# Kernel tuning notes

Measured on AMD Instinct MI355X. Metric: run time of the kernel, lower is better.

Reference implementation:

```python
import jax, jax.numpy as jnp
import numpy as np

N = 50000       # nodes
E = 800000      # edges (avg degree 16)
H = 64          # hidden_channels
T = 4           # towers
F = H // T      # per-tower channels (divide_input=True) = 16
NAGG, NSC = 5, 3
# degree histogram passed as mol_deg -> avg log-degree scaler constant (as in PyG PNAConv)
MOL_DEG = np.array([0, 5, 15, 30, 25, 15, 7, 2, 1], dtype=np.float64)
_bins = np.arange(len(MOL_DEG))
AVG_LOG = float((np.log(_bins + 1.0) * MOL_DEG).sum() / MOL_DEG.sum())


def setup_inputs() -> dict:
    key = jax.random.key(0)
    ks = jax.random.split(key, 12)
    g = lambda k, shp, s=0.1: jax.random.normal(k, shp, dtype=jnp.float32) * s
    return {
        "atom_x": g(ks[0], (N, H), 1.0),
        "bond_emb": g(ks[1], (5, H)),                      # Embedding(5, H)
        "edge_w": g(ks[2], (H, F)), "edge_b": jnp.zeros((F,), jnp.float32),
        "pre_w1": g(ks[3], (T, 3 * F, F)), "pre_b1": jnp.zeros((T, F), jnp.float32),
        "pre_w2": g(ks[4], (T, F, F)), "pre_b2": jnp.zeros((T, F), jnp.float32),
        "post_w1": g(ks[5], (T, (1 + NAGG * NSC) * F, F)), "post_b1": jnp.zeros((T, F), jnp.float32),
        "post_w2": g(ks[6], (T, F, F)), "post_b2": jnp.zeros((T, F), jnp.float32),
        "lin_w": g(ks[7], (H, H)), "lin_b": jnp.zeros((H,), jnp.float32),
        "ln_g": jnp.ones((H,), jnp.float32), "ln_b": jnp.zeros((H,), jnp.float32),
        "bond_x": jax.random.randint(ks[8], (E,), 0, 5),
        "atom_edge_index": jax.random.randint(ks[9], (2, E), 0, N),
    }


def reference(atom_x, bond_emb, edge_w, edge_b, pre_w1, pre_b1, pre_w2, pre_b2,
              post_w1, post_b1, post_w2, post_b2, lin_w, lin_b, ln_g, ln_b,
              bond_x, atom_edge_index):
    src, dst = atom_edge_index[0], atom_edge_index[1]
    # bond encoder + PNA edge encoder (edge_dim -> F_in)
    e = bond_emb[bond_x] @ edge_w + edge_b                       # [E, F]
    xt = atom_x.reshape(N, T, F)                                 # divide_input
    x_j, x_i = xt[src], xt[dst]                                  # [E, T, F]
    et = jnp.broadcast_to(e[:, None, :], (E, T, F))
    h = jnp.concatenate([x_i, x_j, et], axis=-1)                 # [E, T, 3F]
    # per-tower pre-MLP (Linear -> ReLU -> Linear)
    h = jax.nn.relu(jnp.einsum('etf,tfg->etg', h, pre_w1) + pre_b1)
    h = jnp.einsum('etf,tfg->etg', h, pre_w2) + pre_b2           # messages [E, T, F]

    s = jax.ops.segment_sum(h, dst, num_segments=N)
    cnt = jax.ops.segment_sum(jnp.ones((E,), h.dtype), dst, num_segments=N)
    cnt_c = jnp.maximum(cnt, 1.0)[:, None, None]
    mean = s / cnt_c
    mean2 = jax.ops.segment_sum(h * h, dst, num_segments=N) / cnt_c
    std = jnp.sqrt(jax.nn.relu(mean2 - mean * mean) + 1e-5)
    has = (cnt > 0)[:, None, None]
    mn = jnp.where(has, jax.ops.segment_min(h, dst, num_segments=N), 0.0)
    mx = jnp.where(has, jax.ops.segment_max(h, dst, num_segments=N), 0.0)
    agg = jnp.concatenate([s, mean, mn, mx, std], axis=-1)       # [N, T, 5F]

    # degree scalers (deg clamped to 1, as in PyG DegreeScalerAggregation)
    ld = jnp.log(jnp.maximum(cnt, 1.0) + 1.0)[:, None, None]
    agg = jnp.concatenate([agg, agg * (ld / AVG_LOG), agg * (AVG_LOG / ld)], axis=-1)  # [N, T, 15F]

    out = jnp.concatenate([xt, agg], axis=-1)                    # [N, T, 16F]
    # per-tower post-MLP, then mix towers with final Linear
    out = jax.nn.relu(jnp.einsum('ntf,tfg->ntg', out, post_w1) + post_b1)
    out = jnp.einsum('ntf,tfg->ntg', out, post_w2) + post_b2     # [N, T, F]
    out = out.reshape(N, H) @ lin_w + lin_b                      # [N, H]

    # LayerNorm + ReLU + residual (dropout is identity in eval)
    mu = out.mean(-1, keepdims=True)
    var = out.var(-1, keepdims=True)
    ln = (out - mu) / jnp.sqrt(var + 1e-5) * ln_g + ln_b
    return atom_x + jax.nn.relu(ln)
```

## Files before the change

### kernel.cpp

```cpp
#include <hip/hip_runtime.h>
#include <cstdint>

typedef unsigned short u16;

#define AVG_LOG_F 1.4862356961977451f
#define MAXD 64

#define OFF_W2   3072
#define OFF_PW1  4096
#define OFF_PW2  20480
#define OFF_LW   21504
#define OFF_PB1  25600
#define OFF_PB2  25664
#define OFF_QB1  25728
#define OFF_QB2  25792
#define OFF_LB   25856
#define OFF_LG   25920
#define OFF_LBN  25984
#define OFF_EWT  26128
#define IB       26448

__device__ __forceinline__ float bf2f(u16 u) {
    return __uint_as_float(((unsigned)u) << 16);
}
__device__ __forceinline__ u16 f2bf(float f) {
    unsigned u = __float_as_uint(f);
    u += 0x7fffu + ((u >> 16) & 1u);
    return (u16)(u >> 16);
}
__device__ __forceinline__ float rdin(const void* p, long j, int mode) {
    if (mode == 0) return bf2f(((const u16*)p)[j]);
    return ((const float*)p)[j];
}
template <int MODE>
__device__ __forceinline__ void load16c(const void* p, long base, float* o) {
    if (MODE == 0) {
        const u16* q = (const u16*)p + base;
        uint4 a = *(const uint4*)q;
        uint4 b = *(const uint4*)(q + 8);
        o[0]  = __uint_as_float(a.x << 16); o[1]  = __uint_as_float(a.x & 0xffff0000u);
        o[2]  = __uint_as_float(a.y << 16); o[3]  = __uint_as_float(a.y & 0xffff0000u);
        o[4]  = __uint_as_float(a.z << 16); o[5]  = __uint_as_float(a.z & 0xffff0000u);
        o[6]  = __uint_as_float(a.w << 16); o[7]  = __uint_as_float(a.w & 0xffff0000u);
        o[8]  = __uint_as_float(b.x << 16); o[9]  = __uint_as_float(b.x & 0xffff0000u);
        o[10] = __uint_as_float(b.y << 16); o[11] = __uint_as_float(b.y & 0xffff0000u);
        o[12] = __uint_as_float(b.z << 16); o[13] = __uint_as_float(b.z & 0xffff0000u);
        o[14] = __uint_as_float(b.w << 16); o[15] = __uint_as_float(b.w & 0xffff0000u);
    } else {
        const float* q = (const float*)p + base;
        float4 a = *(const float4*)q;
        float4 b = *(const float4*)(q + 4);
        float4 c = *(const float4*)(q + 8);
        float4 d = *(const float4*)(q + 12);
        o[0]=a.x; o[1]=a.y; o[2]=a.z; o[3]=a.w;
        o[4]=b.x; o[5]=b.y; o[6]=b.z; o[7]=b.w;
        o[8]=c.x; o[9]=c.y; o[10]=c.z; o[11]=c.w;
        o[12]=d.x; o[13]=d.y; o[14]=d.z; o[15]=d.w;
    }
}

template <int MODE>
__device__ __forceinline__ void y_loop(const void* ax, const void* pre_w1, float* wsY, float* wsXW,
                                       int Nn, int wave, int nwaves, int l) {
    const int t = l >> 4, g = l & 15;
    float wxi[16], wxj[16];
#pragma unroll
    for (int f = 0; f < 16; f++) {
        wxi[f] = rdin(pre_w1, t * 768 + f * 16 + g, MODE);
        wxj[f] = rdin(pre_w1, t * 768 + (16 + f) * 16 + g, MODE);
    }
    for (int n = wave; n < Nn; n += nwaves) {
        float xj[16];
        load16c<MODE>(ax, (long)n * 64 + t * 16, xj);
        float accY = 0.f, accX = 0.f;
#pragma unroll
        for (int f = 0; f < 16; f++) {
            accY = fmaf(xj[f], wxj[f], accY);
            accX = fmaf(xj[f], wxi[f], accX);
        }
        wsY[(long)n * 64 + l]  = accY;
        wsXW[(long)n * 64 + l] = accX;
    }
}

__global__ __launch_bounds__(256) void k_prep(
    const int* __restrict__ dstp, const int* __restrict__ srcp, const int* __restrict__ bondp,
    const void* bond_emb, const void* edge_w, const void* edge_b,
    const void* pre_w1, const void* pre_b1, const void* pre_w2, const void* pre_b2,
    const void* post_w1, const void* post_b1, const void* post_w2, const void* post_b2,
    const void* lin_w, const void* lin_b, const void* ln_g, const void* ln_b,
    const void* ax, float* wsf, float* wsY, float* wsXW,
    int* __restrict__ cnt, int* __restrict__ pk, int* modep,
    int Nn, int E, int NIB)
{
    int tid = threadIdx.x;
    if ((int)blockIdx.x >= NIB) {
        int e = ((int)blockIdx.x - NIB) * 256 + tid;
        if (e < E) {
            int d = dstp[e];
            int pos = atomicAdd(&cnt[d], 1);
            if (pos < MAXD) pk[d * MAXD + pos] = (srcp[e] << 3) | (bondp[e] & 7);
        }
        return;
    }
    __shared__ int csh;
    __shared__ float ET[80];
    if (tid == 0) csh = 0;
    __syncthreads();
    {
        unsigned v = ((const unsigned*)ax)[tid];
        unsigned lo = v & 0xffffu;
        int ee = (int)((lo >> 7) & 0xff);
        int isbf = (lo == 0u) || (ee >= 110 && ee <= 140);
        atomicAdd(&csh, isbf);
    }
    __syncthreads();
    int mode = (csh >= 192) ? 0 : 1;

    int b = (int)blockIdx.x;
    int gt = b * 256 + tid;
    int gs = NIB * 256;
    if (b == 0 && tid == 0) modep[0] = mode;

    for (int j = gt; j < 1024; j += gs)  wsf[OFF_W2 + j]  = rdin(pre_w2, j, mode);
    for (int j = gt; j < 16384; j += gs) wsf[OFF_PW1 + j] = rdin(post_w1, j, mode);
    for (int j = gt; j < 1024; j += gs)  wsf[OFF_PW2 + j] = rdin(post_w2, j, mode);
    for (int j = gt; j < 4096; j += gs)  wsf[OFF_LW + j]  = rdin(lin_w, j, mode);
    for (int j = gt; j < 64; j += gs) {
        wsf[OFF_PB1 + j] = rdin(pre_b1, j, mode);
        wsf[OFF_PB2 + j] = rdin(pre_b2, j, mode);
        wsf[OFF_QB1 + j] = rdin(post_b1, j, mode);
        wsf[OFF_QB2 + j] = rdin(post_b2, j, mode);
        wsf[OFF_LB + j]  = rdin(lin_b, j, mode);
        wsf[OFF_LG + j]  = rdin(ln_g, j, mode);
        wsf[OFF_LBN + j] = rdin(ln_b, j, mode);
    }
    if (b == 0) {
        if (tid < 80) {
            int bb = tid >> 4, f = tid & 15;
            float acc = rdin(edge_b, f, mode);
            for (int k = 0; k < 64; k++)
                acc = fmaf(rdin(bond_emb, bb * 64 + k, mode), rdin(edge_w, k * 16 + f, mode), acc);
            ET[tid] = acc;
        }
        __syncthreads();
        for (int j = tid; j < 320; j += 256) {
            int bb = j >> 6, ll = j & 63, tt = ll >> 4, gg = ll & 15;
            float acc = rdin(pre_b1, tt * 16 + gg, mode);
#pragma unroll
            for (int f = 0; f < 16; f++)
                acc = fmaf(ET[bb * 16 + f], rdin(pre_w1, tt * 768 + (32 + f) * 16 + gg, mode), acc);
            wsf[OFF_EWT + j] = acc;
        }
    }
    int wave = gt >> 6;
    int nwaves = gs >> 6;
    int l = tid & 63;
    if (mode == 0) y_loop<0>(ax, pre_w1, wsY, wsXW, Nn, wave, nwaves, l);
    else           y_loop<1>(ax, pre_w1, wsY, wsXW, Nn, wave, nwaves, l);
}

__global__ __launch_bounds__(256, 4) void k_node(
    const void* __restrict__ ax, const float* __restrict__ Yp, const float* __restrict__ XWp,
    const int* __restrict__ pk, const int* __restrict__ cnt,
    const float* __restrict__ wsf, void* __restrict__ outp,
    const int* __restrict__ modep, int Nn)
{
    __shared__ float hb[4][16][64];
    __shared__ float zws[4][5][64];
    __shared__ float qp[4][4][3][64];
    __shared__ float xrow[4][64];
    const int w = threadIdx.x >> 6;
    const int l = threadIdx.x & 63;
    const int t = l >> 4;
    const int g = l & 15;
    const int n = blockIdx.x * 4 + w;
    const int mode = modep[0];
    const bool active = (n < Nn);
    const int nn = active ? n : 0;

    const float* W2  = wsf + OFF_W2  + t * 256;
    const float* PW1 = wsf + OFF_PW1 + t * 4096;
    const float* PW2 = wsf + OFF_PW2 + t * 256;

    float w2c[16];
#pragma unroll
    for (int f = 0; f < 16; f++) w2c[f] = W2[f * 16 + g];
    float pb2g = wsf[OFF_PB2 + t * 16 + g];
    float qb1g = wsf[OFF_QB1 + t * 16 + g];
    float qb2g = wsf[OFF_QB2 + t * 16 + g];

    int deg = active ? cnt[nn] : 0;
    if (deg > MAXD) deg = MAXD;

    int   pkvAll = pk[nn * MAXD + l];
    float XWv    = XWp[(long)nn * 64 + l];
    zws[w][0][l] = XWv + wsf[OFF_EWT + 0 * 64 + l];
    zws[w][1][l] = XWv + wsf[OFF_EWT + 1 * 64 + l];
    zws[w][2][l] = XWv + wsf[OFF_EWT + 2 * 64 + l];
    zws[w][3][l] = XWv + wsf[OFF_EWT + 3 * 64 + l];
    zws[w][4][l] = XWv + wsf[OFF_EWT + 4 * 64 + l];
    xrow[w][l]   = rdin(ax, (long)nn * 64 + l, mode);

    float s = 0.f, s2 = 0.f, mn = 3.0e38f, mx = -3.0e38f;

    auto phaseA = [&](int srclane, int k) {
        int v = __builtin_amdgcn_readlane(pkvAll, srclane);
        float yv = Yp[((long)(v >> 3) << 6) + l];
        float zt = zws[w][v & 7][l];
        hb[w][k][l] = fmaxf(yv + zt, 0.f);
    };
    auto phaseB = [&](int k) {
        const float4* hp = (const float4*)&hb[w][k][t * 16];
        float4 h0 = hp[0], h1 = hp[1], h2 = hp[2], h3 = hp[3];
        float m = pb2g;
        m = fmaf(h0.x, w2c[0],  m); m = fmaf(h0.y, w2c[1],  m);
        m = fmaf(h0.z, w2c[2],  m); m = fmaf(h0.w, w2c[3],  m);
        m = fmaf(h1.x, w2c[4],  m); m = fmaf(h1.y, w2c[5],  m);
        m = fmaf(h1.z, w2c[6],  m); m = fmaf(h1.w, w2c[7],  m);
        m = fmaf(h2.x, w2c[8],  m); m = fmaf(h2.y, w2c[9],  m);
        m = fmaf(h2.z, w2c[10], m); m = fmaf(h2.w, w2c[11], m);
        m = fmaf(h3.x, w2c[12], m); m = fmaf(h3.y, w2c[13], m);
        m = fmaf(h3.z, w2c[14], m); m = fmaf(h3.w, w2c[15], m);
        s += m;
        s2 = fmaf(m, m, s2);
        mn = fminf(mn, m);
        mx = fmaxf(mx, m);
    };

#pragma unroll
    for (int kb = 0; kb < MAXD; kb += 16) {
        if (kb >= deg) break;
        int B = deg - kb; if (B > 16) B = 16;
        if (B == 16) {
#pragma unroll
            for (int k = 0; k < 16; k++) phaseA(kb + k, k);
#pragma unroll 4
            for (int k = 0; k < 16; k++) phaseB(k);
        } else {
            for (int k = 0; k < B; k++) phaseA(kb + k, k);
            for (int k = 0; k < B; k++) phaseB(k);
        }
    }

    if (deg == 0) { mn = 0.f; mx = 0.f; }
    float cf = (float)(deg > 0 ? deg : 1);
    float inv = 1.0f / cf;
    float mean = s * inv;
    float var = s2 * inv - mean * mean;
    float sd = sqrtf(fmaxf(var, 0.f) + 1e-5f);
    float ldv = logf(cf + 1.0f);
    float sc1 = ldv * (1.0f / AVG_LOG_F);
    float sc2 = AVG_LOG_F / ldv;

    hb[w][0][l] = s;
    hb[w][1][l] = mean;
    hb[w][2][l] = mn;
    hb[w][3][l] = mx;
    hb[w][4][l] = sd;
    __syncthreads();

    const int F0 = w * 4;
    float q0[4] = {0,0,0,0}, q1[4] = {0,0,0,0}, q2[4] = {0,0,0,0};
    {
        float xa[4][4];
#pragma unroll
        for (int nd = 0; nd < 4; nd++) {
            float4 v = *(const float4*)&xrow[nd][t * 16 + F0];
            xa[nd][0] = v.x; xa[nd][1] = v.y; xa[nd][2] = v.z; xa[nd][3] = v.w;
        }
#pragma unroll
        for (int fi = 0; fi < 4; fi++) {
            float wv = PW1[(F0 + fi) * 16 + g];
#pragma unroll
            for (int nd = 0; nd < 4; nd++) q0[nd] = fmaf(xa[nd][fi], wv, q0[nd]);
        }
    }
#pragma unroll
    for (int a = 0; a < 5; a++) {
        float xa[4][4];
#pragma unroll
        for (int nd = 0; nd < 4; nd++) {
            float4 v = *(const float4*)&hb[nd][a][t * 16 + F0];
            xa[nd][0] = v.x; xa[nd][1] = v.y; xa[nd][2] = v.z; xa[nd][3] = v.w;
        }
        const int rb = 16 + a * 16;
#pragma unroll
        for (int fi = 0; fi < 4; fi++) {
            const int r = (rb + F0 + fi) * 16 + g;
            float w0  = PW1[r];
            float w1  = PW1[r + 80 * 16];
            float w2v = PW1[r + 160 * 16];
#pragma unroll
            for (int nd = 0; nd < 4; nd++) {
                float x = xa[nd][fi];
                q0[nd] = fmaf(x, w0,  q0[nd]);
                q1[nd] = fmaf(x, w1,  q1[nd]);
                q2[nd] = fmaf(x, w2v, q2[nd]);
            }
        }
    }
#pragma unroll
    for (int nd = 0; nd < 4; nd++) {
        qp[w][nd][0][l] = q0[nd];
        qp[w][nd][1][l] = q1[nd];
        qp[w][nd][2][l] = q2[nd];
    }
    __syncthreads();

    {
        float q0s = qp[0][w][0][l] + qp[1][w][0][l] + qp[2][w][0][l] + qp[3][w][0][l];
        float q1s = qp[0][w][1][l] + qp[1][w][1][l] + qp[2][w][1][l] + qp[3][w][1][l];
        float q2s = qp[0][w][2][l] + qp[1][w][2][l] + qp[2][w][2][l] + qp[3][w][2][l];
        float p1 = fmaxf(fmaf(sc2, q2s, fmaf(sc1, q1s, q0s + qb1g)), 0.f);
        hb[w][5][l] = p1;
        float pw2c[16];
#pragma unroll
        for (int f = 0; f < 16; f++) pw2c[f] = PW2[f * 16 + g];
        float m2 = qb2g;
        const float4* pp = (const float4*)&hb[w][5][t * 16];
        float4 p0 = pp[0], r1 = pp[1], r2 = pp[2], r3 = pp[3];
        m2 = fmaf(p0.x, pw2c[0],  m2); m2 = fmaf(p0.y, pw2c[1],  m2);
        m2 = fmaf(p0.z, pw2c[2],  m2); m2 = fmaf(p0.w, pw2c[3],  m2);
        m2 = fmaf(r1.x, pw2c[4],  m2); m2 = fmaf(r1.y, pw2c[5],  m2);
        m2 = fmaf(r1.z, pw2c[6],  m2); m2 = fmaf(r1.w, pw2c[7],  m2);
        m2 = fmaf(r2.x, pw2c[8],  m2); m2 = fmaf(r2.y, pw2c[9],  m2);
        m2 = fmaf(r2.z, pw2c[10], m2); m2 = fmaf(r2.w, pw2c[11], m2);
        m2 = fmaf(r3.x, pw2c[12], m2); m2 = fmaf(r3.y, pw2c[13], m2);
        m2 = fmaf(r3.z, pw2c[14], m2); m2 = fmaf(r3.w, pw2c[15], m2);
        hb[w][6][l] = m2;
    }
    __syncthreads();

    {
        const float* LW = wsf + OFF_LW;
        const int fb = w * 16;
        float lw[4] = {0,0,0,0};
#pragma unroll
        for (int c = 0; c < 4; c++) {
            float pa[4][4];
#pragma unroll
            for (int nd = 0; nd < 4; nd++) {
                float4 v = *(const float4*)&hb[nd][6][fb + 4 * c];
                pa[nd][0] = v.x; pa[nd][1] = v.y; pa[nd][2] = v.z; pa[nd][3] = v.w;
            }
#pragma unroll
            for (int fi = 0; fi < 4; fi++) {
                float wl = LW[(fb + 4 * c + fi) * 64 + l];
#pragma unroll
                for (int nd = 0; nd < 4; nd++) lw[nd] = fmaf(pa[nd][fi], wl, lw[nd]);
            }
        }
#pragma unroll
        for (int nd = 0; nd < 4; nd++) qp[w][nd][0][l] = lw[nd];
    }
    __syncthreads();

    {
        float a = wsf[OFF_LB + l] + qp[0][w][0][l] + qp[1][w][0][l] + qp[2][w][0][l] + qp[3][w][0][l];
        float s1 = a, sq = a * a;
#pragma unroll
        for (int o = 1; o < 64; o <<= 1) { s1 += __shfl_xor(s1, o); sq += __shfl_xor(sq, o); }
        float mu = s1 * (1.0f / 64.0f);
        float varl = sq * (1.0f / 64.0f) - mu * mu;
        float ln = (a - mu) * rsqrtf(varl + 1e-5f) * wsf[OFF_LG + l] + wsf[OFF_LBN + l];
        if (active) {
            long idx = (long)n * 64 + l;
            float res = xrow[w][l] + fmaxf(ln, 0.f);
            if (mode == 0) ((u16*)outp)[idx] = f2bf(res);
            else           ((float*)outp)[idx] = res;
        }
    }
}

extern "C" void kernel_launch(void* const* d_in, const int* in_sizes, int n_in,
                              void* d_out, int out_size, void* d_ws, size_t ws_size,
                              hipStream_t stream) {
    const void* atom_x   = d_in[0];
    const void* bond_emb = d_in[1];
    const void* edge_w   = d_in[2];
    const void* edge_b   = d_in[3];
    const void* pre_w1   = d_in[4];
    const void* pre_b1   = d_in[5];
    const void* pre_w2   = d_in[6];
    const void* pre_b2   = d_in[7];
    const void* post_w1  = d_in[8];
    const void* post_b1  = d_in[9];
    const void* post_w2  = d_in[10];
    const void* post_b2  = d_in[11];
    const void* lin_w    = d_in[12];
    const void* lin_b    = d_in[13];
    const void* ln_g     = d_in[14];
    const void* ln_b     = d_in[15];
    const int* bond_x    = (const int*)d_in[16];
    const int* aei       = (const int*)d_in[17];

    int E  = in_sizes[16];
    int Nn = in_sizes[0] / 64;
    const int* srcp = aei;
    const int* dstp = aei + E;

    float* wsf = (float*)d_ws;
    int*   wsi = (int*)d_ws;

    size_t o = IB;
    int* modep = wsi + o; o += 16;
    int* cnt   = wsi + o; o += Nn;
    o = (o + 63) & ~(size_t)63;
    int* pk    = wsi + o; o += (size_t)Nn * MAXD;
    float* Yp  = (float*)(wsi + o); o += (size_t)Nn * 64;
    float* XWp = (float*)(wsi + o); o += (size_t)Nn * 64;

    const int NIB  = 1600;
    const int SBLK = (E + 255) / 256;

    (void)hipMemsetAsync(cnt, 0, (size_t)Nn * sizeof(int), stream);
    k_prep<<<NIB + SBLK, 256, 0, stream>>>(dstp, srcp, bond_x,
                                           bond_emb, edge_w, edge_b,
                                           pre_w1, pre_b1, pre_w2, pre_b2,
                                           post_w1, post_b1, post_w2, post_b2,
                                           lin_w, lin_b, ln_g, ln_b,
                                           atom_x, wsf, Yp, XWp, cnt, pk, modep, Nn, E, NIB);
    dim3 gn((Nn + 3) / 4, 1, 1);
    k_node<<<gn, 256, 0, stream>>>(atom_x, Yp, XWp, pk, cnt, wsf, d_out, modep, Nn);
}
```

Before: 291.5 us.

## Sort nodes by degree and process eight nodes per block in node kernel

Adds two small kernels that build a degree histogram and a permutation grouping nodes by in-degree. The node kernel then reads node ids through that permutation, so waves in the same block see similar degrees and spend less time idle in the per-edge loop. Blocks grow to 512 threads covering eight nodes, and the post-MLP and final linear work is split across eight waves, with the degree scalers folded into each partial sum before the cross-wave reduction. This costs two extra launches and scattered output writes, and the larger per-thread accumulator arrays may raise register pressure.

```diff
diff --git a/kernel.cpp b/kernel.cpp
--- a/kernel.cpp
+++ b/kernel.cpp
@@ -160,24 +160,66 @@
     else           y_loop<1>(ax, pre_w1, wsY, wsXW, Nn, wave, nwaves, l);
 }
 
-__global__ __launch_bounds__(256, 4) void k_node(
+__global__ __launch_bounds__(256) void k_hist(const int* __restrict__ cnt, int* __restrict__ hist, int Nn)
+{
+    __shared__ int lh[65];
+    int tid = threadIdx.x;
+    if (tid < 65) lh[tid] = 0;
+    __syncthreads();
+    int n = blockIdx.x * 256 + tid;
+    if (n < Nn) {
+        int d = cnt[n]; if (d > 64) d = 64;
+        atomicAdd(&lh[d], 1);
+    }
+    __syncthreads();
+    if (tid < 65 && lh[tid]) atomicAdd(&hist[tid], lh[tid]);
+}
+
+__global__ __launch_bounds__(256) void k_place(const int* __restrict__ cnt, const int* __restrict__ hist,
+                                               int* __restrict__ binfill, int* __restrict__ perm, int Nn)
+{
+    __shared__ int lh[65], lbase[65], hsh[65];
+    int tid = threadIdx.x;
+    if (tid < 65) { lh[tid] = 0; hsh[tid] = hist[tid]; }
+    __syncthreads();
+    int n = blockIdx.x * 256 + tid;
+    int b = 0, lpos = 0;
+    if (n < Nn) {
+        b = cnt[n]; if (b > 64) b = 64;
+        lpos = atomicAdd(&lh[b], 1);
+    }
+    __syncthreads();
+    if (tid < 65) {
+        int c = lh[tid];
+        lbase[tid] = c ? atomicAdd(&binfill[tid], c) : 0;
+    }
+    __syncthreads();
+    if (n < Nn) {
+        int off = 0;
+        for (int i = 0; i < b; i++) off += hsh[i];
+        perm[off + lbase[b] + lpos] = n;
+    }
+}
+
+__global__ __launch_bounds__(512, 4) void k_node(
     const void* __restrict__ ax, const float* __restrict__ Yp, const float* __restrict__ XWp,
-    const int* __restrict__ pk, const int* __restrict__ cnt,
+    const int* __restrict__ pk, const int* __restrict__ cnt, const int* __restrict__ perm,
     const float* __restrict__ wsf, void* __restrict__ outp,
     const int* __restrict__ modep, int Nn)
 {
-    __shared__ float hb[4][16][64];
-    __shared__ float zws[4][5][64];
-    __shared__ float qp[4][4][3][64];
-    __shared__ float xrow[4][64];
+    __shared__ float hb[8][16][64];
+    __shared__ float zws[8][5][64];
+    __shared__ float qp[8][8][64];
+    __shared__ float xrow[8][64];
+    __shared__ float scl1s[8], scl2s[8];
     const int w = threadIdx.x >> 6;
     const int l = threadIdx.x & 63;
     const int t = l >> 4;
     const int g = l & 15;
-    const int n = blockIdx.x * 4 + w;
+    const int slot = blockIdx.x * 8 + w;
     const int mode = modep[0];
-    const bool active = (n < Nn);
-    const int nn = active ? n : 0;
+    const bool active = (slot < Nn);
+    const int nn = active ? perm[slot] : 0;
 
     const float* W2  = wsf + OFF_W2  + t * 256;
     const float* PW1 = wsf + OFF_PW1 + t * 4096;
@@ -238,7 +280,9 @@
 #pragma unroll 4
             for (int k = 0; k < 16; k++) phaseB(k);
         } else {
+#pragma unroll 4
             for (int k = 0; k < B; k++) phaseA(kb + k, k);
+#pragma unroll 4
             for (int k = 0; k < B; k++) phaseB(k);
         }
     }
@@ -258,61 +302,49 @@
     hb[w][2][l] = mn;
     hb[w][3][l] = mx;
     hb[w][4][l] = sd;
-    __syncthreads();
-
-    const int F0 = w * 4;
-    float q0[4] = {0,0,0,0}, q1[4] = {0,0,0,0}, q2[4] = {0,0,0,0};
+    if (l == 0) { scl1s[w] = sc1; scl2s[w] = sc2; }
+    __syncthreads();
+
     {
-        float xa[4][4];
-#pragma unroll
-        for (int nd = 0; nd < 4; nd++) {
-            float4 v = *(const float4*)&xrow[nd][t * 16 + F0];
-            xa[nd][0] = v.x; xa[nd][1] = v.y; xa[nd][2] = v.z; xa[nd][3] = v.w;
-        }
-#pragma unroll
-        for (int fi = 0; fi < 4; fi++) {
-            float wv = PW1[(F0 + fi) * 16 + g];
-#pragma unroll
-            for (int nd = 0; nd < 4; nd++) q0[nd] = fmaf(xa[nd][fi], wv, q0[nd]);
-        }
-    }
-#pragma unroll
-    for (int a = 0; a < 5; a++) {
-        float xa[4][4];
-#pragma unroll
-        for (int nd = 0; nd < 4; nd++) {
-            float4 v = *(const float4*)&hb[nd][a][t * 16 + F0];
-            xa[nd][0] = v.x; xa[nd][1] = v.y; xa[nd][2] = v.z; xa[nd][3] = v.w;
-        }
-        const int rb = 16 + a * 16;
-#pragma unroll
-        for (int fi = 0; fi < 4; fi++) {
-            const int r = (rb + F0 + fi) * 16 + g;
-            float w0  = PW1[r];
-            float w1  = PW1[r + 80 * 16];
-            float w2v = PW1[r + 160 * 16];
-#pragma unroll
-            for (int nd = 0; nd < 4; nd++) {
-                float x = xa[nd][fi];
-                q0[nd] = fmaf(x, w0,  q0[nd]);
-                q1[nd] = fmaf(x, w1,  q1[nd]);
-                q2[nd] = fmaf(x, w2v, q2[nd]);
+        float q0[8], q1[8], q2[8];
+#pragma unroll
+        for (int nd = 0; nd < 8; nd++) { q0[nd] = 0.f; q1[nd] = 0.f; q2[nd] = 0.f; }
+        const int f0 = 2 * w;
+#pragma unroll
+        for (int fi = 0; fi < 2; fi++) {
+            float wv = PW1[(f0 + fi) * 16 + g];
+#pragma unroll
+            for (int nd = 0; nd < 8; nd++)
+                q0[nd] = fmaf(xrow[nd][t * 16 + f0 + fi], wv, q0[nd]);
+        }
+#pragma unroll
+        for (int a = 0; a < 5; a++) {
+#pragma unroll
+            for (int fi = 0; fi < 2; fi++) {
+                const int r = (16 + a * 16 + f0 + fi) * 16 + g;
+                float w0  = PW1[r];
+                float w1  = PW1[r + 1280];
+                float w2v = PW1[r + 2560];
+#pragma unroll
+                for (int nd = 0; nd < 8; nd++) {
+                    float x = hb[nd][a][t * 16 + f0 + fi];
+                    q0[nd] = fmaf(x, w0,  q0[nd]);
+                    q1[nd] = fmaf(x, w1,  q1[nd]);
+                    q2[nd] = fmaf(x, w2v, q2[nd]);
+                }
             }
         }
-    }
-#pragma unroll
-    for (int nd = 0; nd < 4; nd++) {
-        qp[w][nd][0][l] = q0[nd];
-        qp[w][nd][1][l] = q1[nd];
-        qp[w][nd][2][l] = q2[nd];
+#pragma unroll
+        for (int nd = 0; nd < 8; nd++)
+            qp[w][nd][l] = fmaf(scl2s[nd], q2[nd], fmaf(scl1s[nd], q1[nd], q0[nd]));
     }
     __syncthreads();
 
     {
-        float q0s = qp[0][w][0][l] + qp[1][w][0][l] + qp[2][w][0][l] + qp[3][w][0][l];
-        float q1s = qp[0][w][1][l] + qp[1][w][1][l] + qp[2][w][1][l] + qp[3][w][1][l];
-        float q2s = qp[0][w][2][l] + qp[1][w][2][l] + qp[2][w][2][l] + qp[3][w][2][l];
-        float p1 = fmaxf(fmaf(sc2, q2s, fmaf(sc1, q1s, q0s + qb1g)), 0.f);
+        float q = qb1g;
+#pragma unroll
+        for (int ww = 0; ww < 8; ww++) q += qp[ww][w][l];
+        float p1 = fmaxf(q, 0.f);
         hb[w][5][l] = p1;
         float pw2c[16];
 #pragma unroll
@@ -334,13 +366,15 @@
 
     {
         const float* LW = wsf + OFF_LW;
-        const int fb = w * 16;
-        float lw[4] = {0,0,0,0};
-#pragma unroll
-        for (int c = 0; c < 4; c++) {
-            float pa[4][4];
-#pragma unroll
-            for (int nd = 0; nd < 4; nd++) {
+        const int fb = w * 8;
+        float lw[8];
+#pragma unroll
+        for (int nd = 0; nd < 8; nd++) lw[nd] = 0.f;
+#pragma unroll
+        for (int c = 0; c < 2; c++) {
+            float pa[8][4];
+#pragma unroll
+            for (int nd = 0; nd < 8; nd++) {
                 float4 v = *(const float4*)&hb[nd][6][fb + 4 * c];
                 pa[nd][0] = v.x; pa[nd][1] = v.y; pa[nd][2] = v.z; pa[nd][3] = v.w;
             }
@@ -348,16 +382,18 @@
             for (int fi = 0; fi < 4; fi++) {
                 float wl = LW[(fb + 4 * c + fi) * 64 + l];
 #pragma unroll
-                for (int nd = 0; nd < 4; nd++) lw[nd] = fmaf(pa[nd][fi], wl, lw[nd]);
+                for (int nd = 0; nd < 8; nd++) lw[nd] = fmaf(pa[nd][fi], wl, lw[nd]);
             }
         }
 #pragma unroll
-        for (int nd = 0; nd < 4; nd++) qp[w][nd][0][l] = lw[nd];
+        for (int nd = 0; nd < 8; nd++) qp[w][nd][l] = lw[nd];
     }
     __syncthreads();
 
     {
-        float a = wsf[OFF_LB + l] + qp[0][w][0][l] + qp[1][w][0][l] + qp[2][w][0][l] + qp[3][w][0][l];
+        float a = wsf[OFF_LB + l];
+#pragma unroll
+        for (int ww = 0; ww < 8; ww++) a += qp[ww][w][l];
         float s1 = a, sq = a * a;
 #pragma unroll
         for (int o = 1; o < 64; o <<= 1) { s1 += __shfl_xor(s1, o); sq += __shfl_xor(sq, o); }
@@ -365,7 +401,7 @@
         float varl = sq * (1.0f / 64.0f) - mu * mu;
         float ln = (a - mu) * rsqrtf(varl + 1e-5f) * wsf[OFF_LG + l] + wsf[OFF_LBN + l];
         if (active) {
-            long idx = (long)n * 64 + l;
+            long idx = (long)nn * 64 + l;
             float res = xrow[w][l] + fmaxf(ln, 0.f);
             if (mode == 0) ((u16*)outp)[idx] = f2bf(res);
             else           ((float*)outp)[idx] = res;
@@ -404,23 +440,29 @@
     int*   wsi = (int*)d_ws;
 
     size_t o = IB;
-    int* modep = wsi + o; o += 16;
-    int* cnt   = wsi + o; o += Nn;
+    int* modep   = wsi + o; o += 16;
+    int* cnt     = wsi + o; o += Nn;
+    int* hist    = wsi + o; o += 65;
+    int* binfill = wsi + o; o += 65;
     o = (o + 63) & ~(size_t)63;
-    int* pk    = wsi + o; o += (size_t)Nn * MAXD;
-    float* Yp  = (float*)(wsi + o); o += (size_t)Nn * 64;
-    float* XWp = (float*)(wsi + o); o += (size_t)Nn * 64;
+    int* pk      = wsi + o; o += (size_t)Nn * MAXD;
+    float* Yp    = (float*)(wsi + o); o += (size_t)Nn * 64;
+    float* XWp   = (float*)(wsi + o); o += (size_t)Nn * 64;
+    int* perm    = wsi + o; o += Nn;
 
     const int NIB  = 1600;
     const int SBLK = (E + 255) / 256;
-
-    (void)hipMemsetAsync(cnt, 0, (size_t)Nn * sizeof(int), stream);
+    const int NB   = (Nn + 255) / 256;
+
+    (void)hipMemsetAsync(cnt, 0, (size_t)(Nn + 130) * sizeof(int), stream);
     k_prep<<<NIB + SBLK, 256, 0, stream>>>(dstp, srcp, bond_x,
                                            bond_emb, edge_w, edge_b,
                                            pre_w1, pre_b1, pre_w2, pre_b2,
                                            post_w1, post_b1, post_w2, post_b2,
                                            lin_w, lin_b, ln_g, ln_b,
                                            atom_x, wsf, Yp, XWp, cnt, pk, modep, Nn, E, NIB);
-    dim3 gn((Nn + 3) / 4, 1, 1);
-    k_node<<<gn, 256, 0, stream>>>(atom_x, Yp, XWp, pk, cnt, wsf, d_out, modep, Nn);
-}
+    k_hist<<<NB, 256, 0, stream>>>(cnt, hist, Nn);
+    k_place<<<NB, 256, 0, stream>>>(cnt, hist, binfill, perm, Nn);
+    dim3 gn((Nn + 7) / 8, 1, 1);
+    k_node<<<gn, 512, 0, stream>>>(atom_x, Yp, XWp, pk, cnt, perm, wsf, d_out, modep, Nn);
+}
```

Result: slower. 309.1 us (+6.0%).
